# Kernel optimization log

Measured on AMD Instinct MI355X. Metric: run time of the kernel, lower is better.

## Reference

```python
import jax, jax.numpy as jnp
import numpy as np

D_MODEL = 2048
N_HEADS = 16
HEAD_DIM = D_MODEL // N_HEADS


def setup_inputs() -> dict:
    key = jax.random.key(0)
    ks = jax.random.split(key, 6)
    B, T = 4, 2048
    scale = 1.0 / np.sqrt(D_MODEL)
    x = jax.random.normal(ks[0], (B, T, D_MODEL), dtype=jnp.float32)
    wq = jax.random.normal(ks[1], (D_MODEL, D_MODEL), dtype=jnp.float32) * scale
    wk = jax.random.normal(ks[2], (D_MODEL, D_MODEL), dtype=jnp.float32) * scale
    wv = jax.random.normal(ks[3], (D_MODEL, D_MODEL), dtype=jnp.float32) * scale
    wo = jax.random.normal(ks[4], (D_MODEL, D_MODEL), dtype=jnp.float32) * scale
    bo = jnp.zeros((D_MODEL,), dtype=jnp.float32)
    return {"x": x, "wq": wq, "wk": wk, "wv": wv, "wo": wo, "bo": bo}


def reference(x, wq, wk, wv, wo, bo):
    B, T, C = x.shape
    H, Dh = N_HEADS, HEAD_DIM
    # torch nn.Linear: y = x @ W.T
    q = (x @ wq.T).reshape(B, T, H, Dh).transpose(0, 2, 1, 3)  # (B,H,T,Dh)
    k = (x @ wk.T).reshape(B, T, H, Dh).transpose(0, 2, 1, 3)
    v = (x @ wv.T).reshape(B, T, H, Dh).transpose(0, 2, 1, 3)
    scores = jnp.einsum('bhqd,bhkd->bhqk', q, k) / np.sqrt(Dh).astype(np.float32)
    attn = jax.nn.softmax(scores, axis=-1)  # no causal mask in source
    out = jnp.einsum('bhqk,bhkd->bhqd', attn, v)
    out = out.transpose(0, 2, 1, 3).reshape(B, T, C)
    return out @ wo.T + bo
```

## Files before the change

kernel.cpp:

```cpp
#include <hip/hip_runtime.h>
#include <hip/hip_bf16.h>
#include <math.h>

typedef __attribute__((ext_vector_type(8))) __bf16 bf16x8;
typedef __attribute__((ext_vector_type(4))) float floatx4;

__device__ inline unsigned short f2u(float f) {
  __hip_bfloat16 h = __float2bfloat16(f);
  unsigned short u;
  __builtin_memcpy(&u, &h, 2);
  return u;
}

__device__ inline floatx4 mfma16(bf16x8 a, bf16x8 b, floatx4 c) {
  return __builtin_amdgcn_mfma_f32_16x16x32_bf16(a, b, c, 0, 0, 0);
}

__device__ inline void gload_lds16(const unsigned short* g, unsigned short* l) {
  __builtin_amdgcn_global_load_lds(
      (__attribute__((address_space(1))) void*)g,
      (__attribute__((address_space(3))) void*)l,
      16, 0, 0);
}

__global__ __launch_bounds__(256) void castk(const float* __restrict__ in,
                                             unsigned short* __restrict__ out,
                                             int n4, float scale) {
  int i = blockIdx.x * 256 + threadIdx.x;
  if (i >= n4) return;
  const float4 v = reinterpret_cast<const float4*>(in)[i];
  ushort4 o;
  o.x = f2u(v.x * scale);
  o.y = f2u(v.y * scale);
  o.z = f2u(v.z * scale);
  o.w = f2u(v.w * scale);
  reinterpret_cast<ushort4*>(out)[i] = o;
}

__global__ __launch_bounds__(256) void castw4(const float* __restrict__ wq,
                                              const float* __restrict__ wk,
                                              const float* __restrict__ wv,
                                              const float* __restrict__ wo,
                                              unsigned short* __restrict__ oq,
                                              unsigned short* __restrict__ ok,
                                              unsigned short* __restrict__ ov,
                                              unsigned short* __restrict__ oo,
                                              float qscale) {
  const int tensor = blockIdx.x >> 12;
  const int i = (blockIdx.x & 4095) * 256 + threadIdx.x;
  const float* in = tensor == 0 ? wq : tensor == 1 ? wk : tensor == 2 ? wv : wo;
  unsigned short* out = tensor == 0 ? oq : tensor == 1 ? ok : tensor == 2 ? ov : oo;
  const float s = tensor == 0 ? qscale : 1.0f;
  const float4 v = reinterpret_cast<const float4*>(in)[i];
  ushort4 o;
  o.x = f2u(v.x * s);
  o.y = f2u(v.y * s);
  o.z = f2u(v.z * s);
  o.w = f2u(v.w * s);
  reinterpret_cast<ushort4*>(out)[i] = o;
}

template <int OUT>
__global__ __launch_bounds__(512, 2)
void gemm256(const unsigned short* __restrict__ A,
             const unsigned short* __restrict__ B,
             unsigned short* __restrict__ Cb,
             float* __restrict__ Cf,
             const float* __restrict__ bias,
             int M, int N, int K) {
  extern __shared__ unsigned short lds[];
  const int t = threadIdx.x;
  const int w = t >> 6;
  const int l = t & 63;
  const int wm = w >> 2;
  const int wn = w & 3;
  const int fr = l & 15;
  const int fkb = l >> 4;
  const int key = fr & 7;
  const int sslot = (l & 7) ^ (l >> 3);

  const int m0 = blockIdx.y * 256;
  const int n0 = blockIdx.x * 256;
  const int T = K >> 6;

  auto stage = [&](const unsigned short* G, int rb, int kt2, int h, int ldsbase) {
    const int d2 = kt2 & 1;
    const int rt = h * 128 + w * 16 + (l >> 3);
    const unsigned short* s0 = G + (size_t)(rb + rt) * K + kt2 * 64 + sslot * 8;
    unsigned short* dst = lds + ldsbase + d2 * 16384 + h * 8192 + w * 1024;
    gload_lds16(s0, dst);
    gload_lds16(s0 + (size_t)8 * K, dst + 512);
  };

  floatx4 acc[8][4];
#pragma unroll
  for (int m = 0; m < 8; m++)
#pragma unroll
    for (int n = 0; n < 4; n++) acc[m][n] = (floatx4){0.f, 0.f, 0.f, 0.f};

  stage(A, m0, 0, 0, 0);
  stage(A, m0, 0, 1, 0);
  stage(B, n0, 0, 0, 32768);
  stage(B, n0, 0, 1, 32768);
  if (1 < T) {
    stage(B, n0, 1, 0, 32768);
    stage(B, n0, 1, 1, 32768);
    asm volatile("s_waitcnt vmcnt(4)" ::: "memory");
  } else {
    asm volatile("s_waitcnt vmcnt(0)" ::: "memory");
  }
  __builtin_amdgcn_s_barrier();

#define GPHASE(q, STAGE_STMT)                                               \
  {                                                                         \
    bf16x8 a00 = *reinterpret_cast<const bf16x8*>(                          \
        Ab + (wm * 128 + (2 * (q)) * 16 + fr) * 64 + ((fkb ^ key)) * 8);    \
    bf16x8 a01 = *reinterpret_cast<const bf16x8*>(                          \
        Ab + (wm * 128 + (2 * (q)) * 16 + fr) * 64 + (((4 + fkb) ^ key)) * 8); \
    bf16x8 a10 = *reinterpret_cast<const bf16x8*>(                          \
        Ab + (wm * 128 + (2 * (q) + 1) * 16 + fr) * 64 + ((fkb ^ key)) * 8);\
    bf16x8 a11 = *reinterpret_cast<const bf16x8*>(                          \
        Ab + (wm * 128 + (2 * (q) + 1) * 16 + fr) * 64 + (((4 + fkb) ^ key)) * 8); \
    STAGE_STMT;                                                             \
    __builtin_amdgcn_s_barrier();                                           \
    asm volatile("s_waitcnt lgkmcnt(0)");                                   \
    __builtin_amdgcn_s_setprio(1);                                          \
    _Pragma("unroll")                                                       \
    for (int n = 0; n < 4; n++) {                                           \
      acc[2 * (q)][n] = mfma16(a00, bfr[0][n], acc[2 * (q)][n]);            \
      acc[2 * (q)][n] = mfma16(a01, bfr[1][n], acc[2 * (q)][n]);            \
      acc[2 * (q) + 1][n] = mfma16(a10, bfr[0][n], acc[2 * (q) + 1][n]);    \
      acc[2 * (q) + 1][n] = mfma16(a11, bfr[1][n], acc[2 * (q) + 1][n]);    \
    }                                                                       \
    __builtin_amdgcn_s_setprio(0);                                          \
    __builtin_amdgcn_s_barrier();                                           \
  }

  for (int kt = 0; kt < T; ++kt) {
    const int d = kt & 1;
    const unsigned short* Ab = lds + d * 16384;
    const unsigned short* Bb = lds + 32768 + d * 16384;

    bf16x8 bfr[2][4];
#pragma unroll
    for (int kk = 0; kk < 2; kk++)
#pragma unroll
      for (int n = 0; n < 4; n++)
        bfr[kk][n] = *reinterpret_cast<const bf16x8*>(
            Bb + (wn * 64 + n * 16 + fr) * 64 + (((kk * 4 + fkb) ^ key)) * 8);

    GPHASE(0, if (kt + 1 < T) stage(A, m0, kt + 1, 0, 0));
    GPHASE(1, if (kt + 1 < T) stage(A, m0, kt + 1, 1, 0));
    GPHASE(2, if (kt + 2 < T) stage(B, n0, kt + 2, 0, 32768));
    GPHASE(3, {
      if (kt + 2 < T) {
        stage(B, n0, kt + 2, 1, 32768);
        asm volatile("s_waitcnt vmcnt(4)" ::: "memory");
      } else {
        asm volatile("s_waitcnt vmcnt(0)" ::: "memory");
      }
    });
  }
#undef GPHASE

  const int er = (l >> 4) * 4;
  const int ec = l & 15;
#pragma unroll
  for (int m = 0; m < 8; m++) {
#pragma unroll
    for (int n = 0; n < 4; n++) {
      const int col = n0 + wn * 64 + n * 16 + ec;
      if (OUT == 2) {
        const int hv = col >> 7, dh = col & 127;
        const int row0 = m0 + wm * 128 + m * 16 + er;
        const int bb = row0 >> 11;
        const int t0 = row0 & 2047;
        unsigned short* vp =
            Cb + (((size_t)(bb * 16 + hv)) * 128 + dh) * 2048 + t0;
#pragma unroll
        for (int r = 0; r < 4; r++) vp[r] = f2u(acc[m][n][r]);
      } else {
#pragma unroll
        for (int r = 0; r < 4; r++) {
          const int row = m0 + wm * 128 + m * 16 + er + r;
          if (OUT == 1) {
            Cf[(size_t)row * N + col] = acc[m][n][r] + bias[col];
          } else {
            Cb[(size_t)row * N + col] = f2u(acc[m][n][r]);
          }
        }
      }
    }
  }
}

__global__ __launch_bounds__(256, 2)
void attn_kernel(const unsigned short* __restrict__ Y2,
                 const unsigned short* __restrict__ Vtg,
                 unsigned short* __restrict__ att) {
  __shared__ unsigned short Kt[64 * 128];
  __shared__ unsigned short Vt[128 * 64];
  __shared__ unsigned short Pl[4][32 * 72];

  const int t = threadIdx.x;
  const int w = t >> 6;
  const int l = t & 63;
  const int bid = blockIdx.x;
  const int bh = bid & 63;
  const int qt = bid >> 6;
  const int b = bh >> 4;
  const int h = bh & 15;

  const size_t ybase = (size_t)b * 2048 * 4096 + (size_t)h * 128;
  const unsigned short* Qp = Y2 + ybase;
  const unsigned short* Kp = Y2 + ybase + 2048;
  const unsigned short* Vp = Vtg + (size_t)bh * 128 * 2048;

  const int fr = l & 15;
  const int fkb = l >> 4;
  const int key = fr & 7;

  const int ksr = t >> 4;
  const int ksl = (t & 15) ^ (ksr & 7);
  const unsigned short* Ksrc = Kp + (size_t)ksr * 4096 + ksl * 8;

  const int vsr = t >> 3;
  const int vsl = (t & 7) ^ (vsr & 7);
  const unsigned short* Vsrc = Vp + (size_t)vsr * 2048 + vsl * 8;

  bf16x8 qf[2][4];
#pragma unroll
  for (int i = 0; i < 2; i++)
#pragma unroll
    for (int kk = 0; kk < 4; kk++)
      qf[i][kk] = *reinterpret_cast<const bf16x8*>(
          &Qp[(size_t)(qt * 128 + w * 32 + i * 16 + fr) * 4096 + kk * 32 + fkb * 8]);

  floatx4 oacc[2][8];
#pragma unroll
  for (int i = 0; i < 2; i++)
#pragma unroll
    for (int nt = 0; nt < 8; nt++) oacc[i][nt] = (floatx4){0.f, 0.f, 0.f, 0.f};
  float mrun[2][4], lsum[2][4];
#pragma unroll
  for (int i = 0; i < 2; i++)
#pragma unroll
    for (int r = 0; r < 4; r++) {
      mrun[i][r] = -INFINITY;
      lsum[i][r] = 0.f;
    }

  unsigned short* Pw = &Pl[w][0];

#pragma unroll
  for (int c = 0; c < 4; c++)
    gload_lds16(Ksrc + (size_t)c * 16 * 4096, &Kt[c * 2048 + w * 512]);
#pragma unroll
  for (int c = 0; c < 4; c++)
    gload_lds16(Vsrc + (size_t)c * 32 * 2048, &Vt[c * 2048 + w * 512]);
  __syncthreads();

  for (int kv = 0; kv < 2048; kv += 64) {
    floatx4 sacc[2][4];
#pragma unroll
    for (int i = 0; i < 2; i++)
#pragma unroll
      for (int nt = 0; nt < 4; nt++) sacc[i][nt] = (floatx4){0.f, 0.f, 0.f, 0.f};
#pragma unroll
    for (int nt = 0; nt < 4; nt++) {
#pragma unroll
      for (int kk = 0; kk < 4; kk++) {
        bf16x8 kf = *reinterpret_cast<const bf16x8*>(
            &Kt[((nt * 16 + fr) * 16 + ((kk * 4 + fkb) ^ key)) * 8]);
        sacc[0][nt] = mfma16(qf[0][kk], kf, sacc[0][nt]);
        sacc[1][nt] = mfma16(qf[1][kk], kf, sacc[1][nt]);
      }
    }

    float mx4[2][4];
    float dmax = -INFINITY;
#pragma unroll
    for (int i = 0; i < 2; i++)
#pragma unroll
      for (int r = 0; r < 4; r++) {
        mx4[i][r] = fmaxf(fmaxf(sacc[i][0][r], sacc[i][1][r]),
                          fmaxf(sacc[i][2][r], sacc[i][3][r]));
        dmax = fmaxf(dmax, mx4[i][r] - mrun[i][r]);
      }
    if (__any(dmax > 11.5f)) {
#pragma unroll
      for (int i = 0; i < 2; i++)
#pragma unroll
        for (int r = 0; r < 4; r++) {
          float mx = mx4[i][r];
          mx = fmaxf(mx, __shfl_xor(mx, 1));
          mx = fmaxf(mx, __shfl_xor(mx, 2));
          mx = fmaxf(mx, __shfl_xor(mx, 4));
          mx = fmaxf(mx, __shfl_xor(mx, 8));
          const float mn = fmaxf(mrun[i][r], mx);
          const float alpha = exp2f(mrun[i][r] - mn);
          mrun[i][r] = mn;
          lsum[i][r] *= alpha;
#pragma unroll
          for (int nt = 0; nt < 8; nt++) oacc[i][nt][r] *= alpha;
        }
    }
#pragma unroll
    for (int i = 0; i < 2; i++)
#pragma unroll
      for (int r = 0; r < 4; r++) {
        const float m = mrun[i][r];
        const float p0 = exp2f(sacc[i][0][r] - m);
        const float p1 = exp2f(sacc[i][1][r] - m);
        const float p2 = exp2f(sacc[i][2][r] - m);
        const float p3 = exp2f(sacc[i][3][r] - m);
        lsum[i][r] += (p0 + p1) + (p2 + p3);
        const int pr = i * 16 + fkb * 4 + r;
        Pw[pr * 72 + fr] = f2u(p0);
        Pw[pr * 72 + 16 + fr] = f2u(p1);
        Pw[pr * 72 + 32 + fr] = f2u(p2);
        Pw[pr * 72 + 48 + fr] = f2u(p3);
      }

    __syncthreads();

    if (kv + 64 < 2048) {
#pragma unroll
      for (int c = 0; c < 4; c++)
        gload_lds16(Ksrc + (size_t)(kv + 64 + c * 16) * 4096,
                    &Kt[c * 2048 + w * 512]);
    }

    bf16x8 pf[2][2];
#pragma unroll
    for (int i = 0; i < 2; i++) {
      pf[i][0] = *reinterpret_cast<const bf16x8*>(&Pw[(i * 16 + fr) * 72 + fkb * 8]);
      pf[i][1] = *reinterpret_cast<const bf16x8*>(&Pw[(i * 16 + fr) * 72 + 32 + fkb * 8]);
    }
#pragma unroll
    for (int nt = 0; nt < 8; nt++) {
      const unsigned short* vr = &Vt[(nt * 16 + fr) * 64];
      bf16x8 vf0 = *reinterpret_cast<const bf16x8*>(vr + (fkb ^ key) * 8);
      bf16x8 vf1 = *reinterpret_cast<const bf16x8*>(vr + ((fkb + 4) ^ key) * 8);
#pragma unroll
      for (int i = 0; i < 2; i++) {
        oacc[i][nt] = mfma16(pf[i][0], vf0, oacc[i][nt]);
        oacc[i][nt] = mfma16(pf[i][1], vf1, oacc[i][nt]);
      }
    }

    __syncthreads();

    if (kv + 64 < 2048) {
#pragma unroll
      for (int c = 0; c < 4; c++)
        gload_lds16(Vsrc + (size_t)c * 32 * 2048 + (kv + 64),
                    &Vt[c * 2048 + w * 512]);
    }
  }

#pragma unroll
  for (int i = 0; i < 2; i++) {
#pragma unroll
    for (int r = 0; r < 4; r++) {
      float s = lsum[i][r];
      s += __shfl_xor(s, 1);
      s += __shfl_xor(s, 2);
      s += __shfl_xor(s, 4);
      s += __shfl_xor(s, 8);
      const float inv = 1.0f / s;
      const int row = qt * 128 + w * 32 + i * 16 + fkb * 4 + r;
      unsigned short* op = att + ((size_t)b * 2048 + row) * 2048 + h * 128 + fr;
#pragma unroll
      for (int nt = 0; nt < 8; nt++) op[nt * 16] = f2u(oacc[i][nt][r] * inv);
    }
  }
}

extern "C" void kernel_launch(void* const* d_in, const int* in_sizes, int n_in,
                              void* d_out, int out_size, void* d_ws, size_t ws_size,
                              hipStream_t stream) {
  const float* x = (const float*)d_in[0];
  const float* wq = (const float*)d_in[1];
  const float* wk = (const float*)d_in[2];
  const float* wv = (const float*)d_in[3];
  const float* wo = (const float*)d_in[4];
  const float* bo = (const float*)d_in[5];

  unsigned short* ws = (unsigned short*)d_ws;
  unsigned short* x16 = ws;
  unsigned short* wqkv16 = x16 + 16777216;
  unsigned short* wo16 = wqkv16 + 12582912;
  unsigned short* Y2 = wo16 + 4194304;
  unsigned short* Vtg = Y2 + 33554432;
  unsigned short* att16 = Vtg + 16777216;

  const float sscale = 0.12751744900765256f;

  hipFuncSetAttribute(reinterpret_cast<const void*>(gemm256<0>),
                      hipFuncAttributeMaxDynamicSharedMemorySize, 131072);
  hipFuncSetAttribute(reinterpret_cast<const void*>(gemm256<1>),
                      hipFuncAttributeMaxDynamicSharedMemorySize, 131072);
  hipFuncSetAttribute(reinterpret_cast<const void*>(gemm256<2>),
                      hipFuncAttributeMaxDynamicSharedMemorySize, 131072);

  castk<<<16384, 256, 0, stream>>>(x, x16, 4194304, 1.0f);
  castw4<<<16384, 256, 0, stream>>>(wq, wk, wv, wo,
                                    wqkv16, wqkv16 + 4194304,
                                    wqkv16 + 8388608, wo16, sscale);

  dim3 gqk(16, 32);
  gemm256<0><<<gqk, 512, 131072, stream>>>(x16, wqkv16, Y2, nullptr, nullptr,
                                           8192, 4096, 2048);
  dim3 gv(8, 32);
  gemm256<2><<<gv, 512, 131072, stream>>>(x16, wqkv16 + 8388608, Vtg, nullptr,
                                          nullptr, 8192, 2048, 2048);

  attn_kernel<<<1024, 256, 0, stream>>>(Y2, Vtg, att16);

  dim3 go(8, 32);
  gemm256<1><<<go, 512, 131072, stream>>>(att16, wo16, nullptr, (float*)d_out,
                                          bo, 8192, 2048, 2048);
}
```

Measured before the change: 483.5 us.

## Remap GEMM workgroups across XCDs and permute V/P layouts for wider stores

New measurement: 489.4 us. Within noise of the previous version (+1.2%).

```diff
diff --git a/kernel.cpp b/kernel.cpp
--- a/kernel.cpp
+++ b/kernel.cpp
@@ -79,8 +79,13 @@
   const int key = fr & 7;
   const int sslot = (l & 7) ^ (l >> 3);
 
-  const int m0 = blockIdx.y * 256;
-  const int n0 = blockIdx.x * 256;
+  const int nwg = gridDim.x;
+  const int orig = blockIdx.x;
+  const int wgid = (orig & 7) * (nwg >> 3) + (orig >> 3);
+  const int gxm1 = (N >> 8) - 1;
+  const int gxsh = __popc(gxm1);
+  const int m0 = (wgid >> gxsh) * 256;
+  const int n0 = (wgid & gxm1) * 256;
   const int T = K >> 6;
 
   auto stage = [&](const unsigned short* G, int rb, int kt2, int h, int ldsbase) {
@@ -175,10 +180,13 @@
         const int row0 = m0 + wm * 128 + m * 16 + er;
         const int bb = row0 >> 11;
         const int t0 = row0 & 2047;
+        const int blk = t0 & ~63;
+        const int within = t0 & 63;
+        const int c0 = ((within & 15) << 2) | ((within >> 4) & 3);
         unsigned short* vp =
-            Cb + (((size_t)(bb * 16 + hv)) * 128 + dh) * 2048 + t0;
-#pragma unroll
-        for (int r = 0; r < 4; r++) vp[r] = f2u(acc[m][n][r]);
+            Cb + (((size_t)(bb * 16 + hv)) * 128 + dh) * 2048 + blk + c0;
+#pragma unroll
+        for (int r = 0; r < 4; r++) vp[4 * r] = f2u(acc[m][n][r]);
       } else {
 #pragma unroll
         for (int r = 0; r < 4; r++) {
@@ -316,10 +324,12 @@
         const float p3 = exp2f(sacc[i][3][r] - m);
         lsum[i][r] += (p0 + p1) + (p2 + p3);
         const int pr = i * 16 + fkb * 4 + r;
-        Pw[pr * 72 + fr] = f2u(p0);
-        Pw[pr * 72 + 16 + fr] = f2u(p1);
-        Pw[pr * 72 + 32 + fr] = f2u(p2);
-        Pw[pr * 72 + 48 + fr] = f2u(p3);
+        ushort4 pk;
+        pk.x = f2u(p0);
+        pk.y = f2u(p1);
+        pk.z = f2u(p2);
+        pk.w = f2u(p3);
+        *reinterpret_cast<ushort4*>(&Pw[pr * 72 + 4 * fr]) = pk;
       }
 
     __syncthreads();
@@ -409,16 +419,13 @@
                                     wqkv16, wqkv16 + 4194304,
                                     wqkv16 + 8388608, wo16, sscale);
 
-  dim3 gqk(16, 32);
-  gemm256<0><<<gqk, 512, 131072, stream>>>(x16, wqkv16, Y2, nullptr, nullptr,
+  gemm256<0><<<512, 512, 131072, stream>>>(x16, wqkv16, Y2, nullptr, nullptr,
                                            8192, 4096, 2048);
-  dim3 gv(8, 32);
-  gemm256<2><<<gv, 512, 131072, stream>>>(x16, wqkv16 + 8388608, Vtg, nullptr,
-                                          nullptr, 8192, 2048, 2048);
+  gemm256<2><<<256, 512, 131072, stream>>>(x16, wqkv16 + 8388608, Vtg, nullptr,
+                                           nullptr, 8192, 2048, 2048);
 
   attn_kernel<<<1024, 256, 0, stream>>>(Y2, Vtg, att16);
 
-  dim3 go(8, 32);
-  gemm256<1><<<go, 512, 131072, stream>>>(att16, wo16, nullptr, (float*)d_out,
-                                          bo, 8192, 2048, 2048);
-}
+  gemm256<1><<<256, 512, 131072, stream>>>(att16, wo16, nullptr, (float*)d_out,
+                                           bo, 8192, 2048, 2048);
+}
```

## Stage V-transpose epilogue through LDS and pack P stores with permuted key order

Applied to the files above, without the earlier changes.

Result: faster. 463.5 us (-4.1%).

```diff
diff --git a/kernel.cpp b/kernel.cpp
--- a/kernel.cpp
+++ b/kernel.cpp
@@ -4,6 +4,7 @@
 
 typedef __attribute__((ext_vector_type(8))) __bf16 bf16x8;
 typedef __attribute__((ext_vector_type(4))) float floatx4;
+typedef __attribute__((ext_vector_type(8))) unsigned short ushort8v;
 
 __device__ inline unsigned short f2u(float f) {
   __hip_bfloat16 h = __float2bfloat16(f);
@@ -163,23 +164,50 @@
   }
 #undef GPHASE
 
-  const int er = (l >> 4) * 4;
-  const int ec = l & 15;
-#pragma unroll
-  for (int m = 0; m < 8; m++) {
-#pragma unroll
-    for (int n = 0; n < 4; n++) {
-      const int col = n0 + wn * 64 + n * 16 + ec;
-      if (OUT == 2) {
-        const int hv = col >> 7, dh = col & 127;
-        const int row0 = m0 + wm * 128 + m * 16 + er;
-        const int bb = row0 >> 11;
-        const int t0 = row0 & 2047;
-        unsigned short* vp =
-            Cb + (((size_t)(bb * 16 + hv)) * 128 + dh) * 2048 + t0;
-#pragma unroll
-        for (int r = 0; r < 4; r++) vp[r] = f2u(acc[m][n][r]);
-      } else {
+  if (OUT == 2) {
+    unsigned short* TB = lds + w * (64 * 68);
+    const int ec = l & 15;
+    const int hv = (n0 + wn * 64) >> 7;
+    const int bb = (m0 + wm * 128) >> 11;
+    const int s = l & 7;
+    const int dgrp = l >> 3;
+#pragma unroll
+    for (int h2 = 0; h2 < 2; h2++) {
+#pragma unroll
+      for (int mm = 0; mm < 4; mm++) {
+#pragma unroll
+        for (int n = 0; n < 4; n++) {
+#pragma unroll
+          for (int r = 0; r < 4; r++) {
+            const int tau = mm * 16 + (l >> 4) * 4 + r;
+            TB[tau * 68 + n * 16 + ec] = f2u(acc[h2 * 4 + mm][n][r]);
+          }
+        }
+      }
+      const int tbase = ((m0 + wm * 128) & 2047) + h2 * 64;
+#pragma unroll
+      for (int u8 = 0; u8 < 8; u8++) {
+        const int dh = dgrp + 8 * u8;
+        ushort8v buf;
+#pragma unroll
+        for (int e = 0; e < 8; e++) {
+          const int tau = 16 * (e & 3) + 2 * s + (e >> 2);
+          buf[e] = TB[tau * 68 + dh];
+        }
+        unsigned short* vp = Cb +
+            (((size_t)(bb * 16 + hv)) * 128 + (wn & 1) * 64 + dh) * 2048 +
+            tbase + 8 * s;
+        *reinterpret_cast<ushort8v*>(vp) = buf;
+      }
+    }
+  } else {
+    const int er = (l >> 4) * 4;
+    const int ec = l & 15;
+#pragma unroll
+    for (int m = 0; m < 8; m++) {
+#pragma unroll
+      for (int n = 0; n < 4; n++) {
+        const int col = n0 + wn * 64 + n * 16 + ec;
 #pragma unroll
         for (int r = 0; r < 4; r++) {
           const int row = m0 + wm * 128 + m * 16 + er + r;
@@ -316,10 +344,12 @@
         const float p3 = exp2f(sacc[i][3][r] - m);
         lsum[i][r] += (p0 + p1) + (p2 + p3);
         const int pr = i * 16 + fkb * 4 + r;
-        Pw[pr * 72 + fr] = f2u(p0);
-        Pw[pr * 72 + 16 + fr] = f2u(p1);
-        Pw[pr * 72 + 32 + fr] = f2u(p2);
-        Pw[pr * 72 + 48 + fr] = f2u(p3);
+        ushort4 pk;
+        pk.x = f2u(p0);
+        pk.y = f2u(p1);
+        pk.z = f2u(p2);
+        pk.w = f2u(p3);
+        *reinterpret_cast<ushort4*>(&Pw[pr * 72 + 4 * fr]) = pk;
       }
 
     __syncthreads();
```
